# Kernel tuning notes

Hardware: AMD Instinct MI355X
Metric: run time of the kernel (lower is better)

## Reference

```python
import jax, jax.numpy as jnp
import numpy as np

N_NODES = 50000


def binarize(w):
    # straight-through sign binarization (forward: sign, backward: identity)
    return w + jax.lax.stop_gradient(jnp.sign(w) - w)


def sage_conv(x, src, dst, w_l, b_l, w_r, num_nodes):
    # PyG SAGEConv with mean aggregation:
    # out[i] = lin_l(mean_{j in N(i)} x[j]) + lin_r(x[i])
    msgs = x[src]  # [E, F] gather from source nodes
    agg = jax.ops.segment_sum(msgs, dst, num_segments=num_nodes)  # [N, F]
    deg = jax.ops.segment_sum(jnp.ones_like(dst, dtype=x.dtype), dst,
                              num_segments=num_nodes)
    agg = agg / jnp.maximum(deg, 1.0)[:, None]
    return agg @ w_l.T + b_l + x @ w_r.T


def setup_inputs() -> dict:
    key = jax.random.key(0)
    ks = jax.random.split(key, 9)
    in_dim, hid, out_dim = 96, 128, 64
    x = jax.random.normal(ks[0], (N_NODES, in_dim), dtype=jnp.float32)
    edge_index = jax.random.randint(ks[1], (2, 800000), 0, N_NODES, dtype=jnp.int64)
    s1 = 1.0 / np.sqrt(in_dim)
    s2 = 1.0 / np.sqrt(hid)
    w1_l = jax.random.uniform(ks[2], (hid, in_dim), minval=-s1, maxval=s1)
    b1 = jax.random.uniform(ks[3], (hid,), minval=-s1, maxval=s1)
    w1_r = jax.random.uniform(ks[4], (hid, in_dim), minval=-s1, maxval=s1)
    w2_l = jax.random.uniform(ks[5], (out_dim, hid), minval=-s2, maxval=s2)
    b2 = jax.random.uniform(ks[6], (out_dim,), minval=-s2, maxval=s2)
    w2_r = jax.random.uniform(ks[7], (out_dim, hid), minval=-s2, maxval=s2)
    return {"x": x, "edge_index": edge_index, "w1_l": w1_l, "b1": b1,
            "w1_r": w1_r, "w2_l": w2_l, "b2": b2, "w2_r": w2_r}


def reference(x, edge_index, w1_l, b1, w1_r, w2_l, b2, w2_r):
    src, dst = edge_index[0], edge_index[1]
    h = sage_conv(x, src, dst, binarize(w1_l), b1, binarize(w1_r), N_NODES)
    h = jax.nn.relu(h)
    out = sage_conv(h, src, dst, binarize(w2_l), b2, binarize(w2_r), N_NODES)
    return jnp.squeeze(out, axis=-1) if out.shape[-1] == 1 else out
```

## Files before the change

kernel.cpp:

```cpp
#include <hip/hip_runtime.h>
#include <cstdint>
#include <cstddef>


#define N_NODES 50000
#define IN_DIM 96
#define HID 128
#define OUT_DIM 64

typedef __attribute__((ext_vector_type(8))) short bf16x8;
typedef __attribute__((ext_vector_type(4))) float f32x4;

static inline size_t alignUp(size_t v, size_t a) { return (v + a - 1) & ~(a - 1); }

__device__ __forceinline__ uint16_t f2bf(float f) {
  uint32_t u = __float_as_uint(f);
  return (uint16_t)((u + 0x7FFF + ((u >> 16) & 1)) >> 16);
}
__device__ __forceinline__ float bflo(uint32_t v) { return __uint_as_float(v << 16); }
__device__ __forceinline__ float bfhi(uint32_t v) { return __uint_as_float(v & 0xFFFF0000u); }

__global__ __launch_bounds__(256) void bucket_count_kernel(const int* __restrict__ dst,
    int* __restrict__ bucketPart, int E) {
  __shared__ int h[256];
  const int t = threadIdx.x;
  h[t] = 0;
  __syncthreads();
  const int stride = gridDim.x * 256;
  for (int i = blockIdx.x * 256 + t; i < E; i += stride)
    atomicAdd(&h[dst[i] >> 8], 1);
  __syncthreads();
  bucketPart[blockIdx.x * 256 + t] = h[t];
}

__global__ __launch_bounds__(256) void bucket_scan_kernel(const int* __restrict__ bucketPart,
    int* __restrict__ bucketBase, int* __restrict__ bucketCursor, int* __restrict__ rowptr,
    int nB, int N) {
  __shared__ int smem[256];
  const int t = threadIdx.x;
  int v = 0;
  for (int b = 0; b < 256; ++b) v += bucketPart[b * 256 + t];
  if (t >= nB) v = 0;
  smem[t] = v;
  __syncthreads();
  for (int off = 1; off < 256; off <<= 1) {
    int u = (t >= off) ? smem[t - off] : 0;
    __syncthreads();
    smem[t] += u;
    __syncthreads();
  }
  if (t < nB) {
    const int excl = smem[t] - v;
    bucketBase[t] = excl;
    bucketCursor[t] = excl;
  }
  if (t == 255) {
    bucketBase[nB] = smem[255];
    rowptr[N] = smem[255];
  }
}

#define SCAT_CHUNK 2048
__global__ __launch_bounds__(256) void bucket_scatter_kernel(const int* __restrict__ src,
    const int* __restrict__ dst, int* __restrict__ bucketCursor,
    uint32_t* __restrict__ bucketBuf, int E) {
  __shared__ int h[256];
  __shared__ int g[256];
  __shared__ int c[256];
  const int t = threadIdx.x;
  const int base = blockIdx.x * SCAT_CHUNK;
  const int end = min(base + SCAT_CHUNK, E);
  h[t] = 0;
  __syncthreads();
  for (int i = base + t; i < end; i += 256)
    atomicAdd(&h[dst[i] >> 8], 1);
  __syncthreads();
  if (h[t]) g[t] = atomicAdd(&bucketCursor[t], h[t]);
  c[t] = 0;
  __syncthreads();
  for (int i = base + t; i < end; i += 256) {
    const int d = dst[i];
    const int b = d >> 8;
    const int ticket = atomicAdd(&c[b], 1);
    bucketBuf[g[b] + ticket] = (uint32_t)src[i] | ((uint32_t)(d & 255) << 16);
  }
}

__global__ __launch_bounds__(256) void bucket_build_kernel(const uint32_t* __restrict__ bucketBuf,
    const int* __restrict__ bucketBase, int* __restrict__ rowptr,
    uint16_t* __restrict__ adj16, int N) {
  __shared__ int h[256];
  __shared__ int s[256];
  __shared__ int cur[256];
  const int t = threadIdx.x;
  const int b = blockIdx.x;
  const int nodeBase = b << 8;
  const int beg = bucketBase[b], end = bucketBase[b + 1];
  const int m = end - beg;
  h[t] = 0;
  __syncthreads();
  for (int i = t; i < m; i += 256)
    atomicAdd(&h[(bucketBuf[beg + i] >> 16) & 255], 1);
  __syncthreads();
  const int d = h[t];
  s[t] = d;
  __syncthreads();
  for (int off = 1; off < 256; off <<= 1) {
    int u = (t >= off) ? s[t - off] : 0;
    __syncthreads();
    s[t] += u;
    __syncthreads();
  }
  const int excl = s[t] - d;
  const int node = nodeBase + t;
  if (node < N) rowptr[node] = beg + excl;
  cur[t] = excl;
  __syncthreads();
  for (int i = t; i < m; i += 256) {
    const uint32_t u = bucketBuf[beg + i];
    const int ld = (u >> 16) & 255;
    const int ticket = atomicAdd(&cur[ld], 1);
    adj16[beg + ticket] = (uint16_t)(u & 0xFFFFu);
  }
}

__device__ __forceinline__ uint16_t sgnbf(float w) {
  return (w > 0.f) ? (uint16_t)0x3F80 : ((w < 0.f) ? (uint16_t)0xBF80 : (uint16_t)0);
}

#define NS1 (128 * 192)
#define NS2 (128 * 128)
__global__ __launch_bounds__(256) void prep_kernel(const float* __restrict__ x,
    const float* __restrict__ w1l, const float* __restrict__ w1r,
    const float* __restrict__ w2l, const float* __restrict__ w2r,
    uint16_t* __restrict__ S1t, uint16_t* __restrict__ S2t,
    uint16_t* __restrict__ xb, int total4) {
  int idx = blockIdx.x * blockDim.x + threadIdx.x;
  if (idx < NS1) {
    int n = idx / 192, k = idx - n * 192;
    float w = (k < 96) ? w1l[n * 96 + k] : w1r[n * 96 + (k - 96)];
    S1t[idx] = sgnbf(w);
  } else if (idx < NS1 + NS2) {
    int i2 = idx - NS1;
    int n = i2 >> 7, k = i2 & 127;
    float w = (n < 64) ? w2l[n * 128 + k] : w2r[(n - 64) * 128 + k];
    S2t[i2] = sgnbf(w);
  } else {
    int i = idx - NS1 - NS2;
    if (i < total4) {
      float4 v = *(const float4*)(x + (size_t)i * 4);
      uint32_t p0 = (uint32_t)f2bf(v.x) | ((uint32_t)f2bf(v.y) << 16);
      uint32_t p1 = (uint32_t)f2bf(v.z) | ((uint32_t)f2bf(v.w) << 16);
      *(uint2*)(xb + (size_t)i * 4) = make_uint2(p0, p1);
    }
  }
}

__global__ __launch_bounds__(256) void agg1_kernel(const uint16_t* __restrict__ xb,
    const uint16_t* __restrict__ adj16, const int* __restrict__ rowptr,
    uint16_t* __restrict__ AGGb, int nNodes) {
  const int sg = threadIdx.x >> 4;
  const int j = threadIdx.x & 15;
  const int n = blockIdx.x * 16 + sg;
  if (n >= nNodes) return;
  const int beg = rowptr[n], end = rowptr[n + 1];
  const bool act = j < 12;
  const int foff = j * 8;
  float a0 = 0.f, a1 = 0.f, a2 = 0.f, a3 = 0.f, a4 = 0.f, a5 = 0.f, a6 = 0.f, a7 = 0.f;

  int e = beg;
  for (; e + 4 <= end; e += 4) {
    const int s0 = adj16[e], s1 = adj16[e + 1], s2 = adj16[e + 2], s3 = adj16[e + 3];
    uint4 v0 = make_uint4(0u,0u,0u,0u), v1 = v0, v2 = v0, v3 = v0;
    if (act) {
      v0 = *(const uint4*)(xb + (size_t)s0 * IN_DIM + foff);
      v1 = *(const uint4*)(xb + (size_t)s1 * IN_DIM + foff);
      v2 = *(const uint4*)(xb + (size_t)s2 * IN_DIM + foff);
      v3 = *(const uint4*)(xb + (size_t)s3 * IN_DIM + foff);
    }
    __builtin_amdgcn_sched_barrier(0);
    a0 += bflo(v0.x) + bflo(v1.x) + bflo(v2.x) + bflo(v3.x);
    a1 += bfhi(v0.x) + bfhi(v1.x) + bfhi(v2.x) + bfhi(v3.x);
    a2 += bflo(v0.y) + bflo(v1.y) + bflo(v2.y) + bflo(v3.y);
    a3 += bfhi(v0.y) + bfhi(v1.y) + bfhi(v2.y) + bfhi(v3.y);
    a4 += bflo(v0.z) + bflo(v1.z) + bflo(v2.z) + bflo(v3.z);
    a5 += bfhi(v0.z) + bfhi(v1.z) + bfhi(v2.z) + bfhi(v3.z);
    a6 += bflo(v0.w) + bflo(v1.w) + bflo(v2.w) + bflo(v3.w);
    a7 += bfhi(v0.w) + bfhi(v1.w) + bfhi(v2.w) + bfhi(v3.w);
  }
  for (; e < end; ++e) {
    const int s = adj16[e];
    uint4 v = make_uint4(0u,0u,0u,0u);
    if (act) v = *(const uint4*)(xb + (size_t)s * IN_DIM + foff);
    a0 += bflo(v.x); a1 += bfhi(v.x);
    a2 += bflo(v.y); a3 += bfhi(v.y);
    a4 += bflo(v.z); a5 += bfhi(v.z);
    a6 += bflo(v.w); a7 += bfhi(v.w);
  }
  if (act) {
    const int d = end - beg;
    const float inv = 1.0f / (float)(d > 1 ? d : 1);
    uint4 o;
    o.x = (uint32_t)f2bf(a0 * inv) | ((uint32_t)f2bf(a1 * inv) << 16);
    o.y = (uint32_t)f2bf(a2 * inv) | ((uint32_t)f2bf(a3 * inv) << 16);
    o.z = (uint32_t)f2bf(a4 * inv) | ((uint32_t)f2bf(a5 * inv) << 16);
    o.w = (uint32_t)f2bf(a6 * inv) | ((uint32_t)f2bf(a7 * inv) << 16);
    *(uint4*)(AGGb + (size_t)n * IN_DIM + foff) = o;
  }
}

__global__ __launch_bounds__(256) void final_kernel(const uint16_t* __restrict__ T2b,
    const float* __restrict__ R2, const uint16_t* __restrict__ adj16,
    const int* __restrict__ rowptr, float* __restrict__ out, int nNodes) {
  const int sg = threadIdx.x >> 4;
  const int j = threadIdx.x & 15;
  const int n = blockIdx.x * 16 + sg;
  if (n >= nNodes) return;
  const int beg = rowptr[n], end = rowptr[n + 1];
  const int foff = j * 4;
  float a0 = 0.f, a1 = 0.f, a2 = 0.f, a3 = 0.f;

  int e = beg;
  for (; e + 4 <= end; e += 4) {
    const int s0 = adj16[e], s1 = adj16[e + 1], s2 = adj16[e + 2], s3 = adj16[e + 3];
    const uint2 v0 = *(const uint2*)(T2b + (size_t)s0 * 64 + foff);
    const uint2 v1 = *(const uint2*)(T2b + (size_t)s1 * 64 + foff);
    const uint2 v2 = *(const uint2*)(T2b + (size_t)s2 * 64 + foff);
    const uint2 v3 = *(const uint2*)(T2b + (size_t)s3 * 64 + foff);
    __builtin_amdgcn_sched_barrier(0);
    a0 += bflo(v0.x) + bflo(v1.x) + bflo(v2.x) + bflo(v3.x);
    a1 += bfhi(v0.x) + bfhi(v1.x) + bfhi(v2.x) + bfhi(v3.x);
    a2 += bflo(v0.y) + bflo(v1.y) + bflo(v2.y) + bflo(v3.y);
    a3 += bfhi(v0.y) + bfhi(v1.y) + bfhi(v2.y) + bfhi(v3.y);
  }
  for (; e < end; ++e) {
    const int s = adj16[e];
    const uint2 v = *(const uint2*)(T2b + (size_t)s * 64 + foff);
    a0 += bflo(v.x); a1 += bfhi(v.x);
    a2 += bflo(v.y); a3 += bfhi(v.y);
  }
  const int d = end - beg;
  const float inv = 1.0f / (float)(d > 1 ? d : 1);
  const float4 r = *(const float4*)(R2 + (size_t)n * 64 + foff);
  float4 o;
  o.x = a0 * inv + r.x;
  o.y = a1 * inv + r.y;
  o.z = a2 * inv + r.z;
  o.w = a3 * inv + r.w;
  *(float4*)(out + (size_t)n * 64 + foff) = o;
}

#define SP1 200
#define SP2 136
#define HP 136
__global__ __launch_bounds__(256) void gemm12_kernel(
    const uint16_t* __restrict__ AGGb, const uint16_t* __restrict__ xb,
    const uint16_t* __restrict__ S1t, const uint16_t* __restrict__ S2t,
    const float* __restrict__ b1, const float* __restrict__ b2,
    uint16_t* __restrict__ T2b, float* __restrict__ R2, int M) {
  __shared__ uint16_t BS[128 * SP1];
  __shared__ uint16_t Hs[64 * HP];
  const int tid = threadIdx.x;
  const int wv = tid >> 6;
  const int lane = tid & 63;
  const int m16 = lane & 15;
  const int quad = lane >> 4;
  const int rowBase = blockIdx.x * 64 + wv * 16;
  int arow = rowBase + m16;
  if (arow >= M) arow = M - 1;
  const int kq = quad * 8;

#pragma unroll
  for (int i = 0; i < 12; ++i) {
    const int idx8 = tid + i * 256;
    const int col = idx8 / 24;
    const int k8 = (idx8 - col * 24) * 8;
    const bf16x8 v = *(const bf16x8*)(S1t + (size_t)idx8 * 8);
    *(bf16x8*)&BS[col * SP1 + k8] = v;
  }
  bf16x8 a1f[6];
#pragma unroll
  for (int s = 0; s < 3; ++s)
    a1f[s] = *(const bf16x8*)(AGGb + (size_t)arow * IN_DIM + s * 32 + kq);
#pragma unroll
  for (int s = 0; s < 3; ++s)
    a1f[3 + s] = *(const bf16x8*)(xb + (size_t)arow * IN_DIM + s * 32 + kq);
  __syncthreads();

  f32x4 acc1[8];
#pragma unroll
  for (int cf = 0; cf < 8; ++cf) acc1[cf] = (f32x4){0.f, 0.f, 0.f, 0.f};
#pragma unroll
  for (int s = 0; s < 6; ++s) {
#pragma unroll
    for (int cf = 0; cf < 8; ++cf) {
      const bf16x8 b = *(const bf16x8*)&BS[(cf * 16 + m16) * SP1 + s * 32 + kq];
      acc1[cf] = __builtin_amdgcn_mfma_f32_16x16x32_bf16(a1f[s], b, acc1[cf], 0, 0, 0);
    }
  }

#pragma unroll
  for (int cf = 0; cf < 8; ++cf) {
    const int col = cf * 16 + m16;
    const float bias = b1[col];
#pragma unroll
    for (int r = 0; r < 4; ++r) {
      const float v = fmaxf(acc1[cf][r] + bias, 0.f);
      Hs[(wv * 16 + quad * 4 + r) * HP + col] = f2bf(v);
    }
  }
  __syncthreads();

#pragma unroll
  for (int i = 0; i < 8; ++i) {
    const int idx8 = tid + i * 256;
    const int col = idx8 >> 4;
    const int k8 = (idx8 & 15) * 8;
    const bf16x8 v = *(const bf16x8*)(S2t + (size_t)idx8 * 8);
    *(bf16x8*)&BS[col * SP2 + k8] = v;
  }
  __syncthreads();

  f32x4 acc2[8];
#pragma unroll
  for (int cf = 0; cf < 8; ++cf) acc2[cf] = (f32x4){0.f, 0.f, 0.f, 0.f};
#pragma unroll
  for (int s = 0; s < 4; ++s) {
    const bf16x8 a = *(const bf16x8*)&Hs[(wv * 16 + m16) * HP + s * 32 + kq];
#pragma unroll
    for (int cf = 0; cf < 8; ++cf) {
      const bf16x8 b = *(const bf16x8*)&BS[(cf * 16 + m16) * SP2 + s * 32 + kq];
      acc2[cf] = __builtin_amdgcn_mfma_f32_16x16x32_bf16(a, b, acc2[cf], 0, 0, 0);
    }
  }

#pragma unroll
  for (int cf = 0; cf < 8; ++cf) {
    const int col = cf * 16 + m16;
#pragma unroll
    for (int r = 0; r < 4; ++r) {
      const int row = rowBase + quad * 4 + r;
      if (row < M) {
        const float v = acc2[cf][r];
        if (col < 64) {
          T2b[(size_t)row * 64 + col] = f2bf(v);
        } else {
          R2[(size_t)row * 64 + (col - 64)] = v + b2[col - 64];
        }
      }
    }
  }
}

extern "C" void kernel_launch(void* const* d_in, const int* in_sizes, int n_in,
                              void* d_out, int out_size, void* d_ws, size_t ws_size,
                              hipStream_t stream) {
  const float* x   = (const float*)d_in[0];
  const int*   ei  = (const int*)d_in[1];
  const float* w1l = (const float*)d_in[2];
  const float* b1  = (const float*)d_in[3];
  const float* w1r = (const float*)d_in[4];
  const float* w2l = (const float*)d_in[5];
  const float* b2  = (const float*)d_in[6];
  const float* w2r = (const float*)d_in[7];
  float* out = (float*)d_out;

  const int N = in_sizes[0] / IN_DIM;
  const int E = in_sizes[1] / 2;
  const int* src = ei;
  const int* dst = ei + E;
  const int NB = (N + 255) >> 8;

  char* p = (char*)d_ws;
  uint16_t* AGGb = (uint16_t*)p; p += alignUp((size_t)N * IN_DIM * sizeof(uint16_t), 256);
  uint16_t* T2b  = (uint16_t*)p; p += alignUp((size_t)N * 64 * sizeof(uint16_t), 256);
  float* R2      = (float*)p;    p += alignUp((size_t)N * 64 * sizeof(float), 256);
  uint16_t* xb = (uint16_t*)p; p += alignUp((size_t)N * IN_DIM * sizeof(uint16_t), 256);
  uint16_t* S1t = (uint16_t*)p; p += alignUp(NS1 * sizeof(uint16_t), 256);
  uint16_t* S2t = (uint16_t*)p; p += alignUp(NS2 * sizeof(uint16_t), 256);
  int* rowptr = (int*)p; p += alignUp((size_t)(N + 1) * sizeof(int), 256);
  uint16_t* adj16 = (uint16_t*)p; p += alignUp((size_t)E * sizeof(uint16_t), 256);
  uint32_t* bucketBuf = (uint32_t*)p; p += alignUp((size_t)E * sizeof(uint32_t), 256);
  int* bucketPart = (int*)p;   p += alignUp(256 * 256 * sizeof(int), 256);
  int* bucketBase = (int*)p;   p += alignUp(257 * sizeof(int), 256);
  int* bucketCursor = (int*)p; p += alignUp(256 * sizeof(int), 256);
  (void)ws_size; (void)n_in; (void)out_size;

  bucket_count_kernel<<<256, 256, 0, stream>>>(dst, bucketPart, E);
  bucket_scan_kernel<<<1, 256, 0, stream>>>(bucketPart, bucketBase, bucketCursor, rowptr, NB, N);
  bucket_scatter_kernel<<<(E + SCAT_CHUNK - 1) / SCAT_CHUNK, 256, 0, stream>>>(
      src, dst, bucketCursor, bucketBuf, E);
  bucket_build_kernel<<<NB, 256, 0, stream>>>(bucketBuf, bucketBase, rowptr, adj16, N);

  const int total4 = N * IN_DIM / 4;
  const int prepThreads = NS1 + NS2 + total4;
  prep_kernel<<<(prepThreads + 255) / 256, 256, 0, stream>>>(x, w1l, w1r, w2l, w2r,
                                                             S1t, S2t, xb, total4);

  const int nodeBlocks16 = (N + 15) / 16;
  agg1_kernel<<<nodeBlocks16, 256, 0, stream>>>(xb, adj16, rowptr, AGGb, N);

  const int gemmBlocks = (N + 63) / 64;
  gemm12_kernel<<<gemmBlocks, 256, 0, stream>>>(AGGb, xb, S1t, S2t, b1, b2, T2b, R2, N);

  final_kernel<<<nodeBlocks16, 256, 0, stream>>>(T2b, R2, adj16, rowptr, out, N);
}
```

Before: 187.9 us.

## Fuse bucket count with prep kernel and unroll gathers to eight edges

Merges the destination-bucket histogram and the weight/feature preparation into one launch. The histogram now uses 64 blocks instead of 256, which also shrinks the partial-count scan. Both aggregation kernels now read neighbor indices as packed 32-bit pairs, after a one-element alignment peel, and issue eight row gathers per iteration instead of four. This cuts one launch and adds memory-level parallelism in the gathers, at the cost of more registers and less parallelism in the histogram.

New measurement: 189.0 us. Within noise of the previous version (+0.6%).

```diff
diff --git a/kernel.cpp b/kernel.cpp
--- a/kernel.cpp
+++ b/kernel.cpp
@@ -7,6 +7,7 @@
 #define IN_DIM 96
 #define HID 128
 #define OUT_DIM 64
+#define CNT_BLOCKS 64
 
 typedef __attribute__((ext_vector_type(8))) short bf16x8;
 typedef __attribute__((ext_vector_type(4))) float f32x4;
@@ -19,18 +20,51 @@
 }
 __device__ __forceinline__ float bflo(uint32_t v) { return __uint_as_float(v << 16); }
 __device__ __forceinline__ float bfhi(uint32_t v) { return __uint_as_float(v & 0xFFFF0000u); }
-
-__global__ __launch_bounds__(256) void bucket_count_kernel(const int* __restrict__ dst,
-    int* __restrict__ bucketPart, int E) {
+__device__ __forceinline__ uint16_t sgnbf(float w) {
+  return (w > 0.f) ? (uint16_t)0x3F80 : ((w < 0.f) ? (uint16_t)0xBF80 : (uint16_t)0);
+}
+
+#define NS1 (128 * 192)
+#define NS2 (128 * 128)
+
+__global__ __launch_bounds__(256) void count_prep_kernel(const int* __restrict__ dst,
+    int* __restrict__ bucketPart, int E,
+    const float* __restrict__ x,
+    const float* __restrict__ w1l, const float* __restrict__ w1r,
+    const float* __restrict__ w2l, const float* __restrict__ w2r,
+    uint16_t* __restrict__ S1t, uint16_t* __restrict__ S2t,
+    uint16_t* __restrict__ xb, int total4) {
   __shared__ int h[256];
   const int t = threadIdx.x;
-  h[t] = 0;
-  __syncthreads();
-  const int stride = gridDim.x * 256;
-  for (int i = blockIdx.x * 256 + t; i < E; i += stride)
-    atomicAdd(&h[dst[i] >> 8], 1);
-  __syncthreads();
-  bucketPart[blockIdx.x * 256 + t] = h[t];
+  if (blockIdx.x < CNT_BLOCKS) {
+    h[t] = 0;
+    __syncthreads();
+    const int stride = CNT_BLOCKS * 256;
+    for (int i = blockIdx.x * 256 + t; i < E; i += stride)
+      atomicAdd(&h[dst[i] >> 8], 1);
+    __syncthreads();
+    bucketPart[blockIdx.x * 256 + t] = h[t];
+  } else {
+    const int idx = (blockIdx.x - CNT_BLOCKS) * 256 + t;
+    if (idx < NS1) {
+      int n = idx / 192, k = idx - n * 192;
+      float w = (k < 96) ? w1l[n * 96 + k] : w1r[n * 96 + (k - 96)];
+      S1t[idx] = sgnbf(w);
+    } else if (idx < NS1 + NS2) {
+      int i2 = idx - NS1;
+      int n = i2 >> 7, k = i2 & 127;
+      float w = (n < 64) ? w2l[n * 128 + k] : w2r[(n - 64) * 128 + k];
+      S2t[i2] = sgnbf(w);
+    } else {
+      int i = idx - NS1 - NS2;
+      if (i < total4) {
+        float4 v = *(const float4*)(x + (size_t)i * 4);
+        uint32_t p0 = (uint32_t)f2bf(v.x) | ((uint32_t)f2bf(v.y) << 16);
+        uint32_t p1 = (uint32_t)f2bf(v.z) | ((uint32_t)f2bf(v.w) << 16);
+        *(uint2*)(xb + (size_t)i * 4) = make_uint2(p0, p1);
+      }
+    }
+  }
 }
 
 __global__ __launch_bounds__(256) void bucket_scan_kernel(const int* __restrict__ bucketPart,
@@ -39,7 +73,7 @@
   __shared__ int smem[256];
   const int t = threadIdx.x;
   int v = 0;
-  for (int b = 0; b < 256; ++b) v += bucketPart[b * 256 + t];
+  for (int b = 0; b < CNT_BLOCKS; ++b) v += bucketPart[b * 256 + t];
   if (t >= nB) v = 0;
   smem[t] = v;
   __syncthreads();
@@ -124,38 +158,6 @@
   }
 }
 
-__device__ __forceinline__ uint16_t sgnbf(float w) {
-  return (w > 0.f) ? (uint16_t)0x3F80 : ((w < 0.f) ? (uint16_t)0xBF80 : (uint16_t)0);
-}
-
-#define NS1 (128 * 192)
-#define NS2 (128 * 128)
-__global__ __launch_bounds__(256) void prep_kernel(const float* __restrict__ x,
-    const float* __restrict__ w1l, const float* __restrict__ w1r,
-    const float* __restrict__ w2l, const float* __restrict__ w2r,
-    uint16_t* __restrict__ S1t, uint16_t* __restrict__ S2t,
-    uint16_t* __restrict__ xb, int total4) {
-  int idx = blockIdx.x * blockDim.x + threadIdx.x;
-  if (idx < NS1) {
-    int n = idx / 192, k = idx - n * 192;
-    float w = (k < 96) ? w1l[n * 96 + k] : w1r[n * 96 + (k - 96)];
-    S1t[idx] = sgnbf(w);
-  } else if (idx < NS1 + NS2) {
-    int i2 = idx - NS1;
-    int n = i2 >> 7, k = i2 & 127;
-    float w = (n < 64) ? w2l[n * 128 + k] : w2r[(n - 64) * 128 + k];
-    S2t[i2] = sgnbf(w);
-  } else {
-    int i = idx - NS1 - NS2;
-    if (i < total4) {
-      float4 v = *(const float4*)(x + (size_t)i * 4);
-      uint32_t p0 = (uint32_t)f2bf(v.x) | ((uint32_t)f2bf(v.y) << 16);
-      uint32_t p1 = (uint32_t)f2bf(v.z) | ((uint32_t)f2bf(v.w) << 16);
-      *(uint2*)(xb + (size_t)i * 4) = make_uint2(p0, p1);
-    }
-  }
-}
-
 __global__ __launch_bounds__(256) void agg1_kernel(const uint16_t* __restrict__ xb,
     const uint16_t* __restrict__ adj16, const int* __restrict__ rowptr,
     uint16_t* __restrict__ AGGb, int nNodes) {
@@ -169,8 +171,58 @@
   float a0 = 0.f, a1 = 0.f, a2 = 0.f, a3 = 0.f, a4 = 0.f, a5 = 0.f, a6 = 0.f, a7 = 0.f;
 
   int e = beg;
-  for (; e + 4 <= end; e += 4) {
-    const int s0 = adj16[e], s1 = adj16[e + 1], s2 = adj16[e + 2], s3 = adj16[e + 3];
+  if ((e & 1) && e < end) {
+    const int s = adj16[e];
+    uint4 v = make_uint4(0u,0u,0u,0u);
+    if (act) v = *(const uint4*)(xb + (size_t)s * IN_DIM + foff);
+    a0 += bflo(v.x); a1 += bfhi(v.x); a2 += bflo(v.y); a3 += bfhi(v.y);
+    a4 += bflo(v.z); a5 += bfhi(v.z); a6 += bflo(v.w); a7 += bfhi(v.w);
+    ++e;
+  }
+  for (; e + 8 <= end; e += 8) {
+    const uint32_t p0 = *(const uint32_t*)(adj16 + e);
+    const uint32_t p1 = *(const uint32_t*)(adj16 + e + 2);
+    const uint32_t p2 = *(const uint32_t*)(adj16 + e + 4);
+    const uint32_t p3 = *(const uint32_t*)(adj16 + e + 6);
+    const int s0 = p0 & 0xFFFF, s1 = p0 >> 16;
+    const int s2 = p1 & 0xFFFF, s3 = p1 >> 16;
+    const int s4 = p2 & 0xFFFF, s5 = p2 >> 16;
+    const int s6 = p3 & 0xFFFF, s7 = p3 >> 16;
+    uint4 v0 = make_uint4(0u,0u,0u,0u), v1 = v0, v2 = v0, v3 = v0;
+    uint4 v4 = v0, v5 = v0, v6 = v0, v7 = v0;
+    if (act) {
+      v0 = *(const uint4*)(xb + (size_t)s0 * IN_DIM + foff);
+      v1 = *(const uint4*)(xb + (size_t)s1 * IN_DIM + foff);
+      v2 = *(const uint4*)(xb + (size_t)s2 * IN_DIM + foff);
+      v3 = *(const uint4*)(xb + (size_t)s3 * IN_DIM + foff);
+      v4 = *(const uint4*)(xb + (size_t)s4 * IN_DIM + foff);
+      v5 = *(const uint4*)(xb + (size_t)s5 * IN_DIM + foff);
+      v6 = *(const uint4*)(xb + (size_t)s6 * IN_DIM + foff);
+      v7 = *(const uint4*)(xb + (size_t)s7 * IN_DIM + foff);
+    }
+    __builtin_amdgcn_sched_barrier(0);
+    a0 += (bflo(v0.x) + bflo(v1.x) + bflo(v2.x) + bflo(v3.x))
+        + (bflo(v4.x) + bflo(v5.x) + bflo(v6.x) + bflo(v7.x));
+    a1 += (bfhi(v0.x) + bfhi(v1.x) + bfhi(v2.x) + bfhi(v3.x))
+        + (bfhi(v4.x) + bfhi(v5.x) + bfhi(v6.x) + bfhi(v7.x));
+    a2 += (bflo(v0.y) + bflo(v1.y) + bflo(v2.y) + bflo(v3.y))
+        + (bflo(v4.y) + bflo(v5.y) + bflo(v6.y) + bflo(v7.y));
+    a3 += (bfhi(v0.y) + bfhi(v1.y) + bfhi(v2.y) + bfhi(v3.y))
+        + (bfhi(v4.y) + bfhi(v5.y) + bfhi(v6.y) + bfhi(v7.y));
+    a4 += (bflo(v0.z) + bflo(v1.z) + bflo(v2.z) + bflo(v3.z))
+        + (bflo(v4.z) + bflo(v5.z) + bflo(v6.z) + bflo(v7.z));
+    a5 += (bfhi(v0.z) + bfhi(v1.z) + bfhi(v2.z) + bfhi(v3.z))
+        + (bfhi(v4.z) + bfhi(v5.z) + bfhi(v6.z) + bfhi(v7.z));
+    a6 += (bflo(v0.w) + bflo(v1.w) + bflo(v2.w) + bflo(v3.w))
+        + (bflo(v4.w) + bflo(v5.w) + bflo(v6.w) + bflo(v7.w));
+    a7 += (bfhi(v0.w) + bfhi(v1.w) + bfhi(v2.w) + bfhi(v3.w))
+        + (bfhi(v4.w) + bfhi(v5.w) + bfhi(v6.w) + bfhi(v7.w));
+  }
+  if (e + 4 <= end) {
+    const uint32_t p0 = *(const uint32_t*)(adj16 + e);
+    const uint32_t p1 = *(const uint32_t*)(adj16 + e + 2);
+    const int s0 = p0 & 0xFFFF, s1 = p0 >> 16;
+    const int s2 = p1 & 0xFFFF, s3 = p1 >> 16;
     uint4 v0 = make_uint4(0u,0u,0u,0u), v1 = v0, v2 = v0, v3 = v0;
     if (act) {
       v0 = *(const uint4*)(xb + (size_t)s0 * IN_DIM + foff);
@@ -187,15 +239,14 @@
     a5 += bfhi(v0.z) + bfhi(v1.z) + bfhi(v2.z) + bfhi(v3.z);
     a6 += bflo(v0.w) + bflo(v1.w) + bflo(v2.w) + bflo(v3.w);
     a7 += bfhi(v0.w) + bfhi(v1.w) + bfhi(v2.w) + bfhi(v3.w);
+    e += 4;
   }
   for (; e < end; ++e) {
     const int s = adj16[e];
     uint4 v = make_uint4(0u,0u,0u,0u);
     if (act) v = *(const uint4*)(xb + (size_t)s * IN_DIM + foff);
-    a0 += bflo(v.x); a1 += bfhi(v.x);
-    a2 += bflo(v.y); a3 += bfhi(v.y);
-    a4 += bflo(v.z); a5 += bfhi(v.z);
-    a6 += bflo(v.w); a7 += bfhi(v.w);
+    a0 += bflo(v.x); a1 += bfhi(v.x); a2 += bflo(v.y); a3 += bfhi(v.y);
+    a4 += bflo(v.z); a5 += bfhi(v.z); a6 += bflo(v.w); a7 += bfhi(v.w);
   }
   if (act) {
     const int d = end - beg;
@@ -221,8 +272,44 @@
   float a0 = 0.f, a1 = 0.f, a2 = 0.f, a3 = 0.f;
 
   int e = beg;
-  for (; e + 4 <= end; e += 4) {
-    const int s0 = adj16[e], s1 = adj16[e + 1], s2 = adj16[e + 2], s3 = adj16[e + 3];
+  if ((e & 1) && e < end) {
+    const int s = adj16[e];
+    const uint2 v = *(const uint2*)(T2b + (size_t)s * 64 + foff);
+    a0 += bflo(v.x); a1 += bfhi(v.x); a2 += bflo(v.y); a3 += bfhi(v.y);
+    ++e;
+  }
+  for (; e + 8 <= end; e += 8) {
+    const uint32_t p0 = *(const uint32_t*)(adj16 + e);
+    const uint32_t p1 = *(const uint32_t*)(adj16 + e + 2);
+    const uint32_t p2 = *(const uint32_t*)(adj16 + e + 4);
+    const uint32_t p3 = *(const uint32_t*)(adj16 + e + 6);
+    const int s0 = p0 & 0xFFFF, s1 = p0 >> 16;
+    const int s2 = p1 & 0xFFFF, s3 = p1 >> 16;
+    const int s4 = p2 & 0xFFFF, s5 = p2 >> 16;
+    const int s6 = p3 & 0xFFFF, s7 = p3 >> 16;
+    const uint2 v0 = *(const uint2*)(T2b + (size_t)s0 * 64 + foff);
+    const uint2 v1 = *(const uint2*)(T2b + (size_t)s1 * 64 + foff);
+    const uint2 v2 = *(const uint2*)(T2b + (size_t)s2 * 64 + foff);
+    const uint2 v3 = *(const uint2*)(T2b + (size_t)s3 * 64 + foff);
+    const uint2 v4 = *(const uint2*)(T2b + (size_t)s4 * 64 + foff);
+    const uint2 v5 = *(const uint2*)(T2b + (size_t)s5 * 64 + foff);
+    const uint2 v6 = *(const uint2*)(T2b + (size_t)s6 * 64 + foff);
+    const uint2 v7 = *(const uint2*)(T2b + (size_t)s7 * 64 + foff);
+    __builtin_amdgcn_sched_barrier(0);
+    a0 += (bflo(v0.x) + bflo(v1.x) + bflo(v2.x) + bflo(v3.x))
+        + (bflo(v4.x) + bflo(v5.x) + bflo(v6.x) + bflo(v7.x));
+    a1 += (bfhi(v0.x) + bfhi(v1.x) + bfhi(v2.x) + bfhi(v3.x))
+        + (bfhi(v4.x) + bfhi(v5.x) + bfhi(v6.x) + bfhi(v7.x));
+    a2 += (bflo(v0.y) + bflo(v1.y) + bflo(v2.y) + bflo(v3.y))
+        + (bflo(v4.y) + bflo(v5.y) + bflo(v6.y) + bflo(v7.y));
+    a3 += (bfhi(v0.y) + bfhi(v1.y) + bfhi(v2.y) + bfhi(v3.y))
+        + (bfhi(v4.y) + bfhi(v5.y) + bfhi(v6.y) + bfhi(v7.y));
+  }
+  if (e + 4 <= end) {
+    const uint32_t p0 = *(const uint32_t*)(adj16 + e);
+    const uint32_t p1 = *(const uint32_t*)(adj16 + e + 2);
+    const int s0 = p0 & 0xFFFF, s1 = p0 >> 16;
+    const int s2 = p1 & 0xFFFF, s3 = p1 >> 16;
     const uint2 v0 = *(const uint2*)(T2b + (size_t)s0 * 64 + foff);
     const uint2 v1 = *(const uint2*)(T2b + (size_t)s1 * 64 + foff);
     const uint2 v2 = *(const uint2*)(T2b + (size_t)s2 * 64 + foff);
@@ -232,12 +319,12 @@
     a1 += bfhi(v0.x) + bfhi(v1.x) + bfhi(v2.x) + bfhi(v3.x);
     a2 += bflo(v0.y) + bflo(v1.y) + bflo(v2.y) + bflo(v3.y);
     a3 += bfhi(v0.y) + bfhi(v1.y) + bfhi(v2.y) + bfhi(v3.y);
+    e += 4;
   }
   for (; e < end; ++e) {
     const int s = adj16[e];
     const uint2 v = *(const uint2*)(T2b + (size_t)s * 64 + foff);
-    a0 += bflo(v.x); a1 += bfhi(v.x);
-    a2 += bflo(v.y); a3 += bfhi(v.y);
+    a0 += bflo(v.x); a1 += bfhi(v.x); a2 += bflo(v.y); a3 += bfhi(v.y);
   }
   const int d = end - beg;
   const float inv = 1.0f / (float)(d > 1 ? d : 1);
@@ -381,22 +468,21 @@
   int* rowptr = (int*)p; p += alignUp((size_t)(N + 1) * sizeof(int), 256);
   uint16_t* adj16 = (uint16_t*)p; p += alignUp((size_t)E * sizeof(uint16_t), 256);
   uint32_t* bucketBuf = (uint32_t*)p; p += alignUp((size_t)E * sizeof(uint32_t), 256);
-  int* bucketPart = (int*)p;   p += alignUp(256 * 256 * sizeof(int), 256);
+  int* bucketPart = (int*)p;   p += alignUp(CNT_BLOCKS * 256 * sizeof(int), 256);
   int* bucketBase = (int*)p;   p += alignUp(257 * sizeof(int), 256);
   int* bucketCursor = (int*)p; p += alignUp(256 * sizeof(int), 256);
   (void)ws_size; (void)n_in; (void)out_size;
 
-  bucket_count_kernel<<<256, 256, 0, stream>>>(dst, bucketPart, E);
+  const int total4 = N * IN_DIM / 4;
+  const int prepThreads = NS1 + NS2 + total4;
+  const int prepBlocks = (prepThreads + 255) / 256;
+  count_prep_kernel<<<CNT_BLOCKS + prepBlocks, 256, 0, stream>>>(
+      dst, bucketPart, E, x, w1l, w1r, w2l, w2r, S1t, S2t, xb, total4);
   bucket_scan_kernel<<<1, 256, 0, stream>>>(bucketPart, bucketBase, bucketCursor, rowptr, NB, N);
   bucket_scatter_kernel<<<(E + SCAT_CHUNK - 1) / SCAT_CHUNK, 256, 0, stream>>>(
       src, dst, bucketCursor, bucketBuf, E);
   bucket_build_kernel<<<NB, 256, 0, stream>>>(bucketBuf, bucketBase, rowptr, adj16, N);
 
-  const int total4 = N * IN_DIM / 4;
-  const int prepThreads = NS1 + NS2 + total4;
-  prep_kernel<<<(prepThreads + 255) / 256, 256, 0, stream>>>(x, w1l, w1r, w2l, w2r,
-                                                             S1t, S2t, xb, total4);
-
   const int nodeBlocks16 = (N + 15) / 16;
   agg1_kernel<<<nodeBlocks16, 256, 0, stream>>>(xb, adj16, rowptr, AGGb, N);
 
```

## Gather int8 per-row quantized features in both aggregations; fuse count with prep

Applied to the files above, without the earlier changes.

Both neighbour-gather passes now read features stored as int8 with a per-row float scale instead of bf16. The input features are quantized in a fused count+prep kernel, and the layer-2 transformed features are quantized in the GEMM epilogue using a cross-lane row max. This halves the bytes per gathered row and adds one scale load per edge, plus wider 8-edge unrolling with paired index loads. The bucket count kernel is merged into the prep launch with fewer count blocks, removing one launch. The change costs accuracy, since 8-bit per-row quantization is coarser than bf16.

Result: slower. 214.1 us (+13.9%).

```diff
diff --git a/kernel.cpp b/kernel.cpp
--- a/kernel.cpp
+++ b/kernel.cpp
@@ -7,6 +7,7 @@
 #define IN_DIM 96
 #define HID 128
 #define OUT_DIM 64
+#define CNT_BLOCKS 64
 
 typedef __attribute__((ext_vector_type(8))) short bf16x8;
 typedef __attribute__((ext_vector_type(4))) float f32x4;
@@ -19,18 +20,80 @@
 }
 __device__ __forceinline__ float bflo(uint32_t v) { return __uint_as_float(v << 16); }
 __device__ __forceinline__ float bfhi(uint32_t v) { return __uint_as_float(v & 0xFFFF0000u); }
-
-__global__ __launch_bounds__(256) void bucket_count_kernel(const int* __restrict__ dst,
-    int* __restrict__ bucketPart, int E) {
+__device__ __forceinline__ uint16_t sgnbf(float w) {
+  return (w > 0.f) ? (uint16_t)0x3F80 : ((w < 0.f) ? (uint16_t)0xBF80 : (uint16_t)0);
+}
+__device__ __forceinline__ float i8f(uint32_t w, int b) {
+  return (float)(int8_t)((w >> (8 * b)) & 0xFF);
+}
+
+#define NS1 (128 * 192)
+#define NS2 (128 * 128)
+
+__global__ __launch_bounds__(256) void count_prep_kernel(const int* __restrict__ dst,
+    int* __restrict__ bucketPart, int E,
+    const float* __restrict__ x,
+    const float* __restrict__ w1l, const float* __restrict__ w1r,
+    const float* __restrict__ w2l, const float* __restrict__ w2r,
+    uint16_t* __restrict__ S1t, uint16_t* __restrict__ S2t,
+    uint16_t* __restrict__ xb, int total4,
+    int8_t* __restrict__ xq, float* __restrict__ xscale, int N) {
   __shared__ int h[256];
   const int t = threadIdx.x;
-  h[t] = 0;
-  __syncthreads();
-  const int stride = gridDim.x * 256;
-  for (int i = blockIdx.x * 256 + t; i < E; i += stride)
-    atomicAdd(&h[dst[i] >> 8], 1);
-  __syncthreads();
-  bucketPart[blockIdx.x * 256 + t] = h[t];
+  if (blockIdx.x < CNT_BLOCKS) {
+    h[t] = 0;
+    __syncthreads();
+    const int stride = CNT_BLOCKS * 256;
+    for (int i = blockIdx.x * 256 + t; i < E; i += stride)
+      atomicAdd(&h[dst[i] >> 8], 1);
+    __syncthreads();
+    bucketPart[blockIdx.x * 256 + t] = h[t];
+    return;
+  }
+  const int idx = (blockIdx.x - CNT_BLOCKS) * 256 + t;
+  if (idx < NS1) {
+    int n = idx / 192, k = idx - n * 192;
+    float w = (k < 96) ? w1l[n * 96 + k] : w1r[n * 96 + (k - 96)];
+    S1t[idx] = sgnbf(w);
+  } else if (idx < NS1 + NS2) {
+    int i2 = idx - NS1;
+    int n = i2 >> 7, k = i2 & 127;
+    float w = (n < 64) ? w2l[n * 128 + k] : w2r[(n - 64) * 128 + k];
+    S2t[i2] = sgnbf(w);
+  } else if (idx < NS1 + NS2 + total4) {
+    int i = idx - NS1 - NS2;
+    float4 v = *(const float4*)(x + (size_t)i * 4);
+    uint32_t p0 = (uint32_t)f2bf(v.x) | ((uint32_t)f2bf(v.y) << 16);
+    uint32_t p1 = (uint32_t)f2bf(v.z) | ((uint32_t)f2bf(v.w) << 16);
+    *(uint2*)(xb + (size_t)i * 4) = make_uint2(p0, p1);
+  } else {
+    const int row = idx - NS1 - NS2 - total4;
+    if (row < N) {
+      const float* xr = x + (size_t)row * IN_DIM;
+      float mx = 0.f;
+      for (int q = 0; q < 24; ++q) {
+        float4 v = *(const float4*)(xr + q * 4);
+        mx = fmaxf(mx, fmaxf(fmaxf(fabsf(v.x), fabsf(v.y)), fmaxf(fabsf(v.z), fabsf(v.w))));
+      }
+      mx = fmaxf(mx, 1e-8f);
+      const float is = 127.f / mx;
+      xscale[row] = mx / 127.f;
+      int8_t* orow = xq + (size_t)row * IN_DIM;
+      for (int g = 0; g < 6; ++g) {
+        uint32_t w[4];
+#pragma unroll
+        for (int c = 0; c < 4; ++c) {
+          float4 v = *(const float4*)(xr + g * 16 + c * 4);
+          uint32_t b0 = (uint32_t)(uint8_t)(int8_t)__float2int_rn(v.x * is);
+          uint32_t b1 = (uint32_t)(uint8_t)(int8_t)__float2int_rn(v.y * is);
+          uint32_t b2 = (uint32_t)(uint8_t)(int8_t)__float2int_rn(v.z * is);
+          uint32_t b3 = (uint32_t)(uint8_t)(int8_t)__float2int_rn(v.w * is);
+          w[c] = b0 | (b1 << 8) | (b2 << 16) | (b3 << 24);
+        }
+        *(uint4*)(orow + g * 16) = make_uint4(w[0], w[1], w[2], w[3]);
+      }
+    }
+  }
 }
 
 __global__ __launch_bounds__(256) void bucket_scan_kernel(const int* __restrict__ bucketPart,
@@ -39,7 +102,7 @@
   __shared__ int smem[256];
   const int t = threadIdx.x;
   int v = 0;
-  for (int b = 0; b < 256; ++b) v += bucketPart[b * 256 + t];
+  for (int b = 0; b < CNT_BLOCKS; ++b) v += bucketPart[b * 256 + t];
   if (t >= nB) v = 0;
   smem[t] = v;
   __syncthreads();
@@ -124,41 +187,9 @@
   }
 }
 
-__device__ __forceinline__ uint16_t sgnbf(float w) {
-  return (w > 0.f) ? (uint16_t)0x3F80 : ((w < 0.f) ? (uint16_t)0xBF80 : (uint16_t)0);
-}
-
-#define NS1 (128 * 192)
-#define NS2 (128 * 128)
-__global__ __launch_bounds__(256) void prep_kernel(const float* __restrict__ x,
-    const float* __restrict__ w1l, const float* __restrict__ w1r,
-    const float* __restrict__ w2l, const float* __restrict__ w2r,
-    uint16_t* __restrict__ S1t, uint16_t* __restrict__ S2t,
-    uint16_t* __restrict__ xb, int total4) {
-  int idx = blockIdx.x * blockDim.x + threadIdx.x;
-  if (idx < NS1) {
-    int n = idx / 192, k = idx - n * 192;
-    float w = (k < 96) ? w1l[n * 96 + k] : w1r[n * 96 + (k - 96)];
-    S1t[idx] = sgnbf(w);
-  } else if (idx < NS1 + NS2) {
-    int i2 = idx - NS1;
-    int n = i2 >> 7, k = i2 & 127;
-    float w = (n < 64) ? w2l[n * 128 + k] : w2r[(n - 64) * 128 + k];
-    S2t[i2] = sgnbf(w);
-  } else {
-    int i = idx - NS1 - NS2;
-    if (i < total4) {
-      float4 v = *(const float4*)(x + (size_t)i * 4);
-      uint32_t p0 = (uint32_t)f2bf(v.x) | ((uint32_t)f2bf(v.y) << 16);
-      uint32_t p1 = (uint32_t)f2bf(v.z) | ((uint32_t)f2bf(v.w) << 16);
-      *(uint2*)(xb + (size_t)i * 4) = make_uint2(p0, p1);
-    }
-  }
-}
-
-__global__ __launch_bounds__(256) void agg1_kernel(const uint16_t* __restrict__ xb,
-    const uint16_t* __restrict__ adj16, const int* __restrict__ rowptr,
-    uint16_t* __restrict__ AGGb, int nNodes) {
+__global__ __launch_bounds__(256) void agg1_kernel(const int8_t* __restrict__ xq,
+    const float* __restrict__ xscale, const uint16_t* __restrict__ adj16,
+    const int* __restrict__ rowptr, uint16_t* __restrict__ AGGb, int nNodes) {
   const int sg = threadIdx.x >> 4;
   const int j = threadIdx.x & 15;
   const int n = blockIdx.x * 16 + sg;
@@ -169,33 +200,47 @@
   float a0 = 0.f, a1 = 0.f, a2 = 0.f, a3 = 0.f, a4 = 0.f, a5 = 0.f, a6 = 0.f, a7 = 0.f;
 
   int e = beg;
-  for (; e + 4 <= end; e += 4) {
-    const int s0 = adj16[e], s1 = adj16[e + 1], s2 = adj16[e + 2], s3 = adj16[e + 3];
-    uint4 v0 = make_uint4(0u,0u,0u,0u), v1 = v0, v2 = v0, v3 = v0;
-    if (act) {
-      v0 = *(const uint4*)(xb + (size_t)s0 * IN_DIM + foff);
-      v1 = *(const uint4*)(xb + (size_t)s1 * IN_DIM + foff);
-      v2 = *(const uint4*)(xb + (size_t)s2 * IN_DIM + foff);
-      v3 = *(const uint4*)(xb + (size_t)s3 * IN_DIM + foff);
+  if ((e & 1) && e < end) {
+    const int s = adj16[e];
+    const float sc = xscale[s];
+    uint2 v = act ? *(const uint2*)(xq + (size_t)s * IN_DIM + foff) : make_uint2(0u, 0u);
+    a0 += sc * i8f(v.x, 0); a1 += sc * i8f(v.x, 1);
+    a2 += sc * i8f(v.x, 2); a3 += sc * i8f(v.x, 3);
+    a4 += sc * i8f(v.y, 0); a5 += sc * i8f(v.y, 1);
+    a6 += sc * i8f(v.y, 2); a7 += sc * i8f(v.y, 3);
+    ++e;
+  }
+  for (; e + 8 <= end; e += 8) {
+    const uint32_t p0 = *(const uint32_t*)(adj16 + e);
+    const uint32_t p1 = *(const uint32_t*)(adj16 + e + 2);
+    const uint32_t p2 = *(const uint32_t*)(adj16 + e + 4);
+    const uint32_t p3 = *(const uint32_t*)(adj16 + e + 6);
+    const int s[8] = {(int)(p0 & 0xFFFF), (int)(p0 >> 16), (int)(p1 & 0xFFFF), (int)(p1 >> 16),
+                      (int)(p2 & 0xFFFF), (int)(p2 >> 16), (int)(p3 & 0xFFFF), (int)(p3 >> 16)};
+    uint2 v[8];
+    float sc[8];
+#pragma unroll
+    for (int u = 0; u < 8; ++u) {
+      sc[u] = xscale[s[u]];
+      v[u] = act ? *(const uint2*)(xq + (size_t)s[u] * IN_DIM + foff) : make_uint2(0u, 0u);
     }
     __builtin_amdgcn_sched_barrier(0);
-    a0 += bflo(v0.x) + bflo(v1.x) + bflo(v2.x) + bflo(v3.x);
-    a1 += bfhi(v0.x) + bfhi(v1.x) + bfhi(v2.x) + bfhi(v3.x);
-    a2 += bflo(v0.y) + bflo(v1.y) + bflo(v2.y) + bflo(v3.y);
-    a3 += bfhi(v0.y) + bfhi(v1.y) + bfhi(v2.y) + bfhi(v3.y);
-    a4 += bflo(v0.z) + bflo(v1.z) + bflo(v2.z) + bflo(v3.z);
-    a5 += bfhi(v0.z) + bfhi(v1.z) + bfhi(v2.z) + bfhi(v3.z);
-    a6 += bflo(v0.w) + bflo(v1.w) + bflo(v2.w) + bflo(v3.w);
-    a7 += bfhi(v0.w) + bfhi(v1.w) + bfhi(v2.w) + bfhi(v3.w);
+#pragma unroll
+    for (int u = 0; u < 8; ++u) {
+      a0 += sc[u] * i8f(v[u].x, 0); a1 += sc[u] * i8f(v[u].x, 1);
+      a2 += sc[u] * i8f(v[u].x, 2); a3 += sc[u] * i8f(v[u].x, 3);
+      a4 += sc[u] * i8f(v[u].y, 0); a5 += sc[u] * i8f(v[u].y, 1);
+      a6 += sc[u] * i8f(v[u].y, 2); a7 += sc[u] * i8f(v[u].y, 3);
+    }
   }
   for (; e < end; ++e) {
     const int s = adj16[e];
-    uint4 v = make_uint4(0u,0u,0u,0u);
-    if (act) v = *(const uint4*)(xb + (size_t)s * IN_DIM + foff);
-    a0 += bflo(v.x); a1 += bfhi(v.x);
-    a2 += bflo(v.y); a3 += bfhi(v.y);
-    a4 += bflo(v.z); a5 += bfhi(v.z);
-    a6 += bflo(v.w); a7 += bfhi(v.w);
+    const float sc = xscale[s];
+    uint2 v = act ? *(const uint2*)(xq + (size_t)s * IN_DIM + foff) : make_uint2(0u, 0u);
+    a0 += sc * i8f(v.x, 0); a1 += sc * i8f(v.x, 1);
+    a2 += sc * i8f(v.x, 2); a3 += sc * i8f(v.x, 3);
+    a4 += sc * i8f(v.y, 0); a5 += sc * i8f(v.y, 1);
+    a6 += sc * i8f(v.y, 2); a7 += sc * i8f(v.y, 3);
   }
   if (act) {
     const int d = end - beg;
@@ -209,9 +254,10 @@
   }
 }
 
-__global__ __launch_bounds__(256) void final_kernel(const uint16_t* __restrict__ T2b,
-    const float* __restrict__ R2, const uint16_t* __restrict__ adj16,
-    const int* __restrict__ rowptr, float* __restrict__ out, int nNodes) {
+__global__ __launch_bounds__(256) void final_kernel(const int8_t* __restrict__ T2q,
+    const float* __restrict__ tscale, const float* __restrict__ R2,
+    const uint16_t* __restrict__ adj16, const int* __restrict__ rowptr,
+    float* __restrict__ out, int nNodes) {
   const int sg = threadIdx.x >> 4;
   const int j = threadIdx.x & 15;
   const int n = blockIdx.x * 16 + sg;
@@ -221,23 +267,39 @@
   float a0 = 0.f, a1 = 0.f, a2 = 0.f, a3 = 0.f;
 
   int e = beg;
-  for (; e + 4 <= end; e += 4) {
-    const int s0 = adj16[e], s1 = adj16[e + 1], s2 = adj16[e + 2], s3 = adj16[e + 3];
-    const uint2 v0 = *(const uint2*)(T2b + (size_t)s0 * 64 + foff);
-    const uint2 v1 = *(const uint2*)(T2b + (size_t)s1 * 64 + foff);
-    const uint2 v2 = *(const uint2*)(T2b + (size_t)s2 * 64 + foff);
-    const uint2 v3 = *(const uint2*)(T2b + (size_t)s3 * 64 + foff);
+  if ((e & 1) && e < end) {
+    const int s = adj16[e];
+    const float sc = tscale[s];
+    const uint32_t v = *(const uint32_t*)(T2q + (size_t)s * 64 + foff);
+    a0 += sc * i8f(v, 0); a1 += sc * i8f(v, 1); a2 += sc * i8f(v, 2); a3 += sc * i8f(v, 3);
+    ++e;
+  }
+  for (; e + 8 <= end; e += 8) {
+    const uint32_t p0 = *(const uint32_t*)(adj16 + e);
+    const uint32_t p1 = *(const uint32_t*)(adj16 + e + 2);
+    const uint32_t p2 = *(const uint32_t*)(adj16 + e + 4);
+    const uint32_t p3 = *(const uint32_t*)(adj16 + e + 6);
+    const int s[8] = {(int)(p0 & 0xFFFF), (int)(p0 >> 16), (int)(p1 & 0xFFFF), (int)(p1 >> 16),
+                      (int)(p2 & 0xFFFF), (int)(p2 >> 16), (int)(p3 & 0xFFFF), (int)(p3 >> 16)};
+    uint32_t v[8];
+    float sc[8];
+#pragma unroll
+    for (int u = 0; u < 8; ++u) {
+      sc[u] = tscale[s[u]];
+      v[u] = *(const uint32_t*)(T2q + (size_t)s[u] * 64 + foff);
+    }
     __builtin_amdgcn_sched_barrier(0);
-    a0 += bflo(v0.x) + bflo(v1.x) + bflo(v2.x) + bflo(v3.x);
-    a1 += bfhi(v0.x) + bfhi(v1.x) + bfhi(v2.x) + bfhi(v3.x);
-    a2 += bflo(v0.y) + bflo(v1.y) + bflo(v2.y) + bflo(v3.y);
-    a3 += bfhi(v0.y) + bfhi(v1.y) + bfhi(v2.y) + bfhi(v3.y);
+#pragma unroll
+    for (int u = 0; u < 8; ++u) {
+      a0 += sc[u] * i8f(v[u], 0); a1 += sc[u] * i8f(v[u], 1);
+      a2 += sc[u] * i8f(v[u], 2); a3 += sc[u] * i8f(v[u], 3);
+    }
   }
   for (; e < end; ++e) {
     const int s = adj16[e];
-    const uint2 v = *(const uint2*)(T2b + (size_t)s * 64 + foff);
-    a0 += bflo(v.x); a1 += bfhi(v.x);
-    a2 += bflo(v.y); a3 += bfhi(v.y);
+    const float sc = tscale[s];
+    const uint32_t v = *(const uint32_t*)(T2q + (size_t)s * 64 + foff);
+    a0 += sc * i8f(v, 0); a1 += sc * i8f(v, 1); a2 += sc * i8f(v, 2); a3 += sc * i8f(v, 3);
   }
   const int d = end - beg;
   const float inv = 1.0f / (float)(d > 1 ? d : 1);
@@ -257,7 +319,7 @@
     const uint16_t* __restrict__ AGGb, const uint16_t* __restrict__ xb,
     const uint16_t* __restrict__ S1t, const uint16_t* __restrict__ S2t,
     const float* __restrict__ b1, const float* __restrict__ b2,
-    uint16_t* __restrict__ T2b, float* __restrict__ R2, int M) {
+    int8_t* __restrict__ T2q, float* __restrict__ tscale, float* __restrict__ R2, int M) {
   __shared__ uint16_t BS[128 * SP1];
   __shared__ uint16_t Hs[64 * HP];
   const int tid = threadIdx.x;
@@ -335,19 +397,31 @@
   }
 
 #pragma unroll
-  for (int cf = 0; cf < 8; ++cf) {
+  for (int r = 0; r < 4; ++r) {
+    float m = 0.f;
+#pragma unroll
+    for (int cf = 0; cf < 4; ++cf) m = fmaxf(m, fabsf(acc2[cf][r]));
+#pragma unroll
+    for (int w = 1; w < 16; w <<= 1) m = fmaxf(m, __shfl_xor(m, w));
+    m = fmaxf(m, 1e-8f);
+    const float is = 127.f / m;
+    const int row = rowBase + quad * 4 + r;
+    if (row < M) {
+#pragma unroll
+      for (int cf = 0; cf < 4; ++cf) {
+        const int q = __float2int_rn(acc2[cf][r] * is);
+        T2q[(size_t)row * 64 + cf * 16 + m16] = (int8_t)q;
+      }
+      if (m16 == 0) tscale[row] = m / 127.f;
+    }
+  }
+#pragma unroll
+  for (int cf = 4; cf < 8; ++cf) {
     const int col = cf * 16 + m16;
 #pragma unroll
     for (int r = 0; r < 4; ++r) {
       const int row = rowBase + quad * 4 + r;
-      if (row < M) {
-        const float v = acc2[cf][r];
-        if (col < 64) {
-          T2b[(size_t)row * 64 + col] = f2bf(v);
-        } else {
-          R2[(size_t)row * 64 + (col - 64)] = v + b2[col - 64];
-        }
-      }
+      if (row < M) R2[(size_t)row * 64 + (col - 64)] = acc2[cf][r] + b2[col - 64];
     }
   }
 }
@@ -373,35 +447,38 @@
 
   char* p = (char*)d_ws;
   uint16_t* AGGb = (uint16_t*)p; p += alignUp((size_t)N * IN_DIM * sizeof(uint16_t), 256);
-  uint16_t* T2b  = (uint16_t*)p; p += alignUp((size_t)N * 64 * sizeof(uint16_t), 256);
-  float* R2      = (float*)p;    p += alignUp((size_t)N * 64 * sizeof(float), 256);
-  uint16_t* xb = (uint16_t*)p; p += alignUp((size_t)N * IN_DIM * sizeof(uint16_t), 256);
-  uint16_t* S1t = (uint16_t*)p; p += alignUp(NS1 * sizeof(uint16_t), 256);
-  uint16_t* S2t = (uint16_t*)p; p += alignUp(NS2 * sizeof(uint16_t), 256);
-  int* rowptr = (int*)p; p += alignUp((size_t)(N + 1) * sizeof(int), 256);
+  int8_t* T2q = (int8_t*)p;      p += alignUp((size_t)N * 64, 256);
+  float* tscale = (float*)p;     p += alignUp((size_t)N * sizeof(float), 256);
+  float* R2 = (float*)p;         p += alignUp((size_t)N * 64 * sizeof(float), 256);
+  uint16_t* xb = (uint16_t*)p;   p += alignUp((size_t)N * IN_DIM * sizeof(uint16_t), 256);
+  int8_t* xq = (int8_t*)p;       p += alignUp((size_t)N * IN_DIM, 256);
+  float* xscale = (float*)p;     p += alignUp((size_t)N * sizeof(float), 256);
+  uint16_t* S1t = (uint16_t*)p;  p += alignUp(NS1 * sizeof(uint16_t), 256);
+  uint16_t* S2t = (uint16_t*)p;  p += alignUp(NS2 * sizeof(uint16_t), 256);
+  int* rowptr = (int*)p;         p += alignUp((size_t)(N + 1) * sizeof(int), 256);
   uint16_t* adj16 = (uint16_t*)p; p += alignUp((size_t)E * sizeof(uint16_t), 256);
   uint32_t* bucketBuf = (uint32_t*)p; p += alignUp((size_t)E * sizeof(uint32_t), 256);
-  int* bucketPart = (int*)p;   p += alignUp(256 * 256 * sizeof(int), 256);
-  int* bucketBase = (int*)p;   p += alignUp(257 * sizeof(int), 256);
-  int* bucketCursor = (int*)p; p += alignUp(256 * sizeof(int), 256);
+  int* bucketPart = (int*)p;     p += alignUp(CNT_BLOCKS * 256 * sizeof(int), 256);
+  int* bucketBase = (int*)p;     p += alignUp(257 * sizeof(int), 256);
+  int* bucketCursor = (int*)p;   p += alignUp(256 * sizeof(int), 256);
   (void)ws_size; (void)n_in; (void)out_size;
 
-  bucket_count_kernel<<<256, 256, 0, stream>>>(dst, bucketPart, E);
+  const int total4 = N * IN_DIM / 4;
+  const int prepThreads = NS1 + NS2 + total4 + N;
+  const int prepBlocks = (prepThreads + 255) / 256;
+  count_prep_kernel<<<CNT_BLOCKS + prepBlocks, 256, 0, stream>>>(
+      dst, bucketPart, E, x, w1l, w1r, w2l, w2r, S1t, S2t, xb, total4, xq, xscale, N);
   bucket_scan_kernel<<<1, 256, 0, stream>>>(bucketPart, bucketBase, bucketCursor, rowptr, NB, N);
   bucket_scatter_kernel<<<(E + SCAT_CHUNK - 1) / SCAT_CHUNK, 256, 0, stream>>>(
       src, dst, bucketCursor, bucketBuf, E);
   bucket_build_kernel<<<NB, 256, 0, stream>>>(bucketBuf, bucketBase, rowptr, adj16, N);
 
-  const int total4 = N * IN_DIM / 4;
-  const int prepThreads = NS1 + NS2 + total4;
-  prep_kernel<<<(prepThreads + 255) / 256, 256, 0, stream>>>(x, w1l, w1r, w2l, w2r,
-                                                             S1t, S2t, xb, total4);
-
   const int nodeBlocks16 = (N + 15) / 16;
-  agg1_kernel<<<nodeBlocks16, 256, 0, stream>>>(xb, adj16, rowptr, AGGb, N);
+  agg1_kernel<<<nodeBlocks16, 256, 0, stream>>>(xq, xscale, adj16, rowptr, AGGb, N);
 
   const int gemmBlocks = (N + 63) / 64;
-  gemm12_kernel<<<gemmBlocks, 256, 0, stream>>>(AGGb, xb, S1t, S2t, b1, b2, T2b, R2, N);
-
-  final_kernel<<<nodeBlocks16, 256, 0, stream>>>(T2b, R2, adj16, rowptr, out, N);
-}
+  gemm12_kernel<<<gemmBlocks, 256, 0, stream>>>(AGGb, xb, S1t, S2t, b1, b2,
+                                                T2q, tscale, R2, N);
+
+  final_kernel<<<nodeBlocks16, 256, 0, stream>>>(T2q, tscale, R2, adj16, rowptr, out, N);
+}
```
